# Kernel tuning notes

Hardware: AMD Instinct MI355X
Metric: run time of the kernel (lower is better)

## Reference

```python
import jax, jax.numpy as jnp
import numpy as np

B = 2048       # batch
N = 256        # num_memory_locations
M = 64         # memory_size
U = 512        # num_units
IN = 10        # num_bits_per_vector + 2
SHIFT = 1      # conv_shift_range
CLIP = 20.0


def setup_inputs() -> dict:
    key = jax.random.key(0)
    ks = jax.random.split(key, 20)
    s = 0.05
    A0 = jax.random.uniform(ks[5], (2, B, N), dtype=jnp.float32)
    A0 = A0 / jnp.sum(A0, axis=-1, keepdims=True)  # distribution-like prev attention
    return {
        'x_t':  jax.random.normal(ks[0], (B, IN), dtype=jnp.float32),
        'H0':   jax.random.normal(ks[1], (B, U), dtype=jnp.float32) * s,
        'C0':   jax.random.normal(ks[2], (B, U), dtype=jnp.float32) * s,
        'm0':   jax.random.normal(ks[3], (B, N, M), dtype=jnp.float32) * s,
        'R0':   jax.random.normal(ks[4], (B, M), dtype=jnp.float32) * s,
        'A0':   A0,
        'Wprep': jax.random.normal(ks[6], (M, U), dtype=jnp.float32) * s,
        'bprep': jnp.zeros((U,), dtype=jnp.float32),
        'Wx':   jax.random.normal(ks[7], (IN + U, 4 * U), dtype=jnp.float32) * s,
        'Wh':   jax.random.normal(ks[8], (U, 4 * U), dtype=jnp.float32) * s,
        'bl':   jnp.zeros((4 * U,), dtype=jnp.float32),
        'Wr':   jax.random.normal(ks[9], (U, M + 6), dtype=jnp.float32) * s,
        'br':   jnp.zeros((M + 6,), dtype=jnp.float32),
        'Ww':   jax.random.normal(ks[10], (U, 3 * M + 6), dtype=jnp.float32) * s,
        'bw':   jnp.zeros((3 * M + 6,), dtype=jnp.float32),
        'Wo':   jax.random.normal(ks[11], (U + M, U), dtype=jnp.float32) * s,
        'bo':   jnp.zeros((U,), dtype=jnp.float32),
    }


def _addressing(head, m_tm1, a_tm1):
    # head: (B, >=M+6); m_tm1: (B,N,M); a_tm1: (B,N)
    k = jnp.tanh(head[:, :M])                                   # (B,M)
    beta = jax.nn.softplus(head[:, M])                          # (B,)
    g = jax.nn.sigmoid(head[:, M + 1])                          # (B,)
    s = jax.nn.softmax(head[:, M + 2:M + 2 + 2 * SHIFT + 1], axis=-1)  # (B,3)
    gamma = jax.nn.softplus(head[:, M + 2 + 2 * SHIFT + 1])     # (B,)
    # cosine similarity content addressing
    ip = jnp.einsum('bnm,bm->bn', m_tm1, k)                     # (B,N)
    k_norm = jnp.sqrt(jnp.sum(k * k, axis=1, keepdims=True))    # (B,1)
    m_norm = jnp.sqrt(jnp.sum(m_tm1 * m_tm1, axis=2))           # (B,N)
    K = ip / (k_norm * m_norm + 1e-8)
    w_c = jax.nn.softmax(beta[:, None] * K, axis=1)             # exp/sum == softmax
    w_g = g[:, None] * w_c + (1.0 - g[:, None]) * a_tm1
    # circular convolution: s placed at offsets [0..SHIFT] and [-SHIFT..-1]
    s_full = jnp.concatenate(
        [s[:, :SHIFT + 1], jnp.zeros((s.shape[0], N - (2 * SHIFT + 1)), s.dtype), s[:, -SHIFT:]],
        axis=1)                                                 # (B,N)
    idx = (jnp.arange(N)[:, None] - jnp.arange(N)[None, :]) % N  # (N,N)
    w_conv = jnp.einsum('bij,bj->bi', s_full[:, idx], w_g)       # w[i]=sum_j w_g[j]*s[(i-j)%N]
    w_sharp = w_conv ** gamma[:, None]
    return w_sharp / jnp.sum(w_sharp, axis=1, keepdims=True)


def reference(x_t, H0, C0, m0, R0, A0, Wprep, bprep, Wx, Wh, bl, Wr, br, Ww, bw, Wo, bo):
    # prep from previous reads
    h = R0 @ Wprep + bprep                                      # (B,U)
    # single-layer LSTM controller
    z = jnp.concatenate([x_t, h], axis=1) @ Wx + H0 @ Wh + bl   # (B,4U)
    i, f, g_, o = jnp.split(z, 4, axis=1)
    c_t = jax.nn.sigmoid(f) * C0 + jax.nn.sigmoid(i) * jnp.tanh(g_)
    h = jax.nn.sigmoid(o) * jnp.tanh(c_t)
    h = jnp.clip(h, -CLIP, CLIP)
    # heads
    r_out = h @ Wr + br                                         # (B, M+6)
    w_out = h @ Ww + bw                                         # (B, 3M+6)
    w_read = _addressing(r_out, m0, A0[0])                      # (B,N)
    w_write = _addressing(w_out, m0, A0[1])                     # (B,N)
    # read from OLD memory (as in original)
    R_t = jnp.einsum('bn,bnm->bm', w_read, m0)                  # (B,M)
    # write: erase + add
    del_v = jax.nn.sigmoid(w_out[:, -2 * M:-M])                 # (B,M)
    add_v = jnp.tanh(w_out[:, -M:])                             # (B,M)
    ww = w_write[:, :, None]                                    # (B,N,1)
    m_t = m0 * (1.0 - ww * del_v[:, None, :]) + ww * add_v[:, None, :]
    y_t = jnp.clip(jnp.concatenate([h, R_t], axis=1) @ Wo + bo, -CLIP, CLIP)
    return (y_t, m_t, R_t, w_read, w_write)
```

## Files before the change

kernel.cpp:

```cpp
#include <hip/hip_runtime.h>


using u16   = unsigned short;
using bfrag = __attribute__((ext_vector_type(8))) short;
using f4    = __attribute__((ext_vector_type(4))) float;

__device__ __forceinline__ float bf2f(u16 s){ union{float f;unsigned u;}v; v.u=((unsigned)s)<<16; return v.f; }
__device__ __forceinline__ u16 f2bf(float f){ union{float f;unsigned u;}v; v.f=f; unsigned r=v.u+0x7fffu+((v.u>>16)&1u); return (u16)(r>>16); }
__device__ __forceinline__ float sigm(float x){ return 1.f/(1.f+expf(-x)); }
__device__ __forceinline__ float softplus_(float x){ return fmaxf(x,0.f)+log1pf(expf(-fabsf(x))); }

__device__ __forceinline__ void gld16(const u16* g, u16* l){
    __builtin_amdgcn_global_load_lds((const __attribute__((address_space(1))) unsigned*)g,
                                     (__attribute__((address_space(3))) unsigned*)l, 16, 0, 0);
}

__global__ __launch_bounds__(256) void k_prep(const float* __restrict__ Wx, const float* __restrict__ Wh,
                                              const float* __restrict__ Wr, const float* __restrict__ Ww,
                                              const float* __restrict__ Wo,
                                              const float* __restrict__ x, const float* __restrict__ H0,
                                              const float* __restrict__ R0, const float* __restrict__ Wprep,
                                              const float* __restrict__ bprep,
                                              u16* __restrict__ Wt_lstm, u16* __restrict__ Wt_h,
                                              u16* __restrict__ Wt_o, u16* __restrict__ Abuf){
    __shared__ float t[32][33];
    int bx = blockIdx.x;
    int tx = threadIdx.x & 31, ty = threadIdx.x >> 5;
    if(bx < 2112){
        int n0 = (bx & 63)*32, k0 = (bx >> 6)*32;
        #pragma unroll
        for(int r=0;r<4;r++){
            int k = k0 + ty*4 + r, n = n0 + tx;
            float v;
            if(k < 522)       v = Wx[k*2048 + n];
            else if(k < 1034) v = Wh[(k-522)*2048 + n];
            else              v = 0.f;
            t[ty*4+r][tx] = v;
        }
        __syncthreads();
        #pragma unroll
        for(int r=0;r<4;r++){
            int n = n0 + ty*4 + r, k = k0 + tx;
            int u = n & 511, gate = n >> 9;
            int np = ((u>>4)<<6) + (gate<<4) + (u&15);
            Wt_lstm[np*1056 + k] = f2bf(t[tx][ty*4+r]);
        }
    } else if(bx < 2304){
        int idx = bx - 2112;
        int n0 = (idx % 12)*32, k0 = (idx / 12)*32;
        #pragma unroll
        for(int r=0;r<4;r++){
            int k = k0 + ty*4 + r, n = n0 + tx;
            float v;
            if(n < 70)        v = Wr[k*70 + n];
            else if(n < 268)  v = Ww[k*198 + (n-70)];
            else              v = 0.f;
            t[ty*4+r][tx] = v;
        }
        __syncthreads();
        #pragma unroll
        for(int r=0;r<4;r++){
            int n = n0 + ty*4 + r, k = k0 + tx;
            Wt_h[n*512 + k] = f2bf(t[tx][ty*4+r]);
        }
    } else if(bx < 2592){
        int idx = bx - 2304;
        int n0 = (idx % 16)*32, k0 = (idx / 16)*32;
        #pragma unroll
        for(int r=0;r<4;r++){
            int k = k0 + ty*4 + r, n = n0 + tx;
            t[ty*4+r][tx] = Wo[k*512 + n];
        }
        __syncthreads();
        #pragma unroll
        for(int r=0;r<4;r++){
            int n = n0 + ty*4 + r, k = k0 + tx;
            Wt_o[n*576 + k] = f2bf(t[tx][ty*4+r]);
        }
    } else {
        int flat = (bx - 2592)*256 + threadIdx.x;
        int b = flat >> 9, u = flat & 511;
        u16* Ab = Abuf + (size_t)b*1056;
        float acc = bprep[u];
        const float* r = R0 + b*64;
        #pragma unroll 8
        for(int m=0;m<64;m++) acc += r[m] * Wprep[m*512+u];
        Ab[10+u] = f2bf(acc);
        Ab[522+u] = f2bf(H0[b*512+u]);
        if(u<10) Ab[u] = f2bf(x[b*10+u]);
        if(u<22) Ab[1034+u] = 0;
    }
}

__device__ __forceinline__ void gemm128(const u16* __restrict__ A, int lda,
                                        const u16* __restrict__ Bt, int ldb,
                                        int bm, int bn, int kiters,
                                        u16* Al, u16* Bl, f4 acc[4][4]){
    int tid = threadIdx.x, w = tid>>6, lane = tid&63, quad = lane>>4, l16 = lane&15;
    int wr = w>>1, wc = w&1;
    f4 z4 = {0.f,0.f,0.f,0.f};
    #pragma unroll
    for(int i=0;i<4;i++)
        #pragma unroll
        for(int j=0;j<4;j++) acc[i][j] = z4;
    int rA0 = tid>>2, kc = tid&3;
    int rA1 = rA0 + 64;
    const u16* ga0 = A  + (size_t)(bm+rA0)*lda + kc*8;
    const u16* ga1 = A  + (size_t)(bm+rA1)*lda + kc*8;
    const u16* gb0 = Bt + (size_t)(bn+rA0)*ldb + kc*8;
    const u16* gb1 = Bt + (size_t)(bn+rA1)*ldb + kc*8;
    u16* lA0 = Al + (w*64)*8;
    u16* lA1 = Al + (256 + w*64)*8;
    u16* lB0 = Bl + (w*64)*8;
    u16* lB1 = Bl + (256 + w*64)*8;
    for(int kt=0; kt<kiters; kt++){
        __syncthreads();
        gld16(ga0, lA0); gld16(ga1, lA1);
        gld16(gb0, lB0); gld16(gb1, lB1);
        ga0 += 32; ga1 += 32; gb0 += 32; gb1 += 32;
        __syncthreads();
        bfrag af[4], bf[4];
        #pragma unroll
        for(int i=0;i<4;i++) af[i] = *(const bfrag*)&Al[(wr*64 + i*16 + l16)*32 + quad*8];
        #pragma unroll
        for(int j=0;j<4;j++) bf[j] = *(const bfrag*)&Bl[(wc*64 + j*16 + l16)*32 + quad*8];
        #pragma unroll
        for(int i=0;i<4;i++)
            #pragma unroll
            for(int j=0;j<4;j++)
                acc[i][j] = __builtin_amdgcn_mfma_f32_16x16x32_bf16(af[i], bf[j], acc[i][j], 0, 0, 0);
    }
}

__global__ __launch_bounds__(256) void k_gemm_lstm(const u16* __restrict__ A, const u16* __restrict__ Wt,
                                                   const float* __restrict__ C0, const float* __restrict__ bl,
                                                   u16* __restrict__ A2){
    __shared__ u16 Al[128*32], Bl[128*32];
    f4 acc[4][4];
    int bm = blockIdx.x*128, bn = blockIdx.y*128;
    gemm128(A, 1056, Wt, 1056, bm, bn, 33, Al, Bl, acc);
    int lane = threadIdx.x&63, quad = lane>>4, l16 = lane&15, w = threadIdx.x>>6;
    int wr = w>>1, wc = w&1;
    int u = (((bn + wc*64)>>6)<<4) + l16;
    float bi = bl[u], bff = bl[512+u], bg = bl[1024+u], bo_ = bl[1536+u];
    #pragma unroll
    for(int i=0;i<4;i++){
        #pragma unroll
        for(int r=0;r<4;r++){
            int b = bm + wr*64 + i*16 + quad*4 + r;
            float zi = acc[i][0][r] + bi;
            float zf = acc[i][1][r] + bff;
            float zg = acc[i][2][r] + bg;
            float zo = acc[i][3][r] + bo_;
            float c  = sigm(zf)*C0[b*512+u] + sigm(zi)*tanhf(zg);
            float hv = sigm(zo)*tanhf(c);
            hv = fminf(fmaxf(hv,-20.f),20.f);
            A2[(size_t)b*576 + u] = f2bf(hv);
        }
    }
}

__global__ __launch_bounds__(256) void k_gemm_heads(const u16* __restrict__ A2, const u16* __restrict__ Wt,
                                                    const float* __restrict__ br, const float* __restrict__ bw,
                                                    float* __restrict__ rout, float* __restrict__ wout){
    __shared__ u16 Al[128*32], Bl[128*32];
    f4 acc[4][4];
    int bm = blockIdx.x*128, bn = blockIdx.y*128;
    gemm128(A2, 576, Wt, 512, bm, bn, 16, Al, Bl, acc);
    int lane = threadIdx.x&63, quad = lane>>4, l16 = lane&15, w = threadIdx.x>>6;
    int wr = w>>1, wc = w&1;
    #pragma unroll
    for(int i=0;i<4;i++){
        #pragma unroll
        for(int j=0;j<4;j++){
            int col = bn + wc*64 + j*16 + l16;
            if(col >= 268) continue;
            #pragma unroll
            for(int r=0;r<4;r++){
                int row = bm + wr*64 + i*16 + quad*4 + r;
                float v = acc[i][j][r];
                if(col < 70) rout[(size_t)row*70 + col]        = v + br[col];
                else         wout[(size_t)row*198 + (col-70)]  = v + bw[col-70];
            }
        }
    }
}

__global__ __launch_bounds__(256) void k_gemm_out(const u16* __restrict__ A2, const u16* __restrict__ Wt,
                                                  const float* __restrict__ bo, float* __restrict__ y){
    __shared__ u16 Al[128*32], Bl[128*32];
    f4 acc[4][4];
    int bm = blockIdx.x*128, bn = blockIdx.y*128;
    gemm128(A2, 576, Wt, 576, bm, bn, 18, Al, Bl, acc);
    int lane = threadIdx.x&63, quad = lane>>4, l16 = lane&15, w = threadIdx.x>>6;
    int wr = w>>1, wc = w&1;
    #pragma unroll
    for(int i=0;i<4;i++){
        #pragma unroll
        for(int j=0;j<4;j++){
            int col = bn + wc*64 + j*16 + l16;
            float bias = bo[col];
            #pragma unroll
            for(int r=0;r<4;r++){
                int row = bm + wr*64 + i*16 + quad*4 + r;
                float v = acc[i][j][r] + bias;
                v = fminf(fmaxf(v,-20.f),20.f);
                y[(size_t)row*512 + col] = v;
            }
        }
    }
}

__global__ __launch_bounds__(256, 4) void k_addr(const float* __restrict__ m0, const float* __restrict__ A0,
                                              const float* __restrict__ rout, const float* __restrict__ wout,
                                              u16* __restrict__ A2,
                                              float* __restrict__ out_mt, float* __restrict__ out_rt,
                                              float* __restrict__ out_wr, float* __restrict__ out_ww){
    __shared__ __align__(16) float kk_s[2][64];
    __shared__ float knorm_s[2];
    __shared__ float sc[2][6];
    __shared__ float ipbuf[3][256];
    __shared__ float wgrr[512];
    __shared__ float wsel[2][256];
    __shared__ __align__(16) float dv[64], avv[64];
    __shared__ float wpart[4][6];
    int tid = threadIdx.x, b = blockIdx.x;
    int lane = tid & 63, w = tid >> 6;
    int g = tid >> 4, c = tid & 15, mc = c*4;

    float a0r = A0[b*256 + tid];
    float a1r = A0[524288 + b*256 + tid];

    float4 v[16];
    const float* mb = m0 + (size_t)b*16384;
    #pragma unroll
    for(int i=0;i<16;i++) v[i] = *(const float4*)(mb + i*1024 + tid*4);

    if(tid < 128){
        int hh = tid >> 6, m = lane;
        float kv = tanhf(hh ? wout[b*198 + m] : rout[b*70 + m]);
        kk_s[hh][m] = kv;
        float s2 = kv*kv;
        #pragma unroll
        for(int o=32;o>0;o>>=1) s2 += __shfl_xor(s2, o, 64);
        if(m == 0) knorm_s[hh] = sqrtf(s2);
    } else if(tid < 192){
        int hh = tid - 128;
        if(hh < 2){
            const float* hd = hh ? (wout + b*198) : (rout + b*70);
            sc[hh][0] = softplus_(hd[64]);
            sc[hh][1] = sigm(hd[65]);
            float e0=hd[66], e1=hd[67], e2=hd[68];
            float mx = fmaxf(e0, fmaxf(e1, e2));
            float x0=expf(e0-mx), x1=expf(e1-mx), x2=expf(e2-mx);
            float ssum = x0+x1+x2;
            sc[hh][2]=x0/ssum; sc[hh][3]=x1/ssum; sc[hh][4]=x2/ssum;
            sc[hh][5] = softplus_(hd[69]);
        }
    } else {
        int m = tid - 192;
        dv[m]  = sigm(wout[b*198 + 70 + m]);
        avv[m] = tanhf(wout[b*198 + 134 + m]);
    }
    __syncthreads();

    {
        float4 ka = *(const float4*)&kk_s[0][mc];
        float4 kb = *(const float4*)&kk_s[1][mc];
        float rip0=0.f, rip1=0.f, rssq=0.f;
        #pragma unroll
        for(int i=0;i<16;i++){
            float4 t = v[i];
            float p0 = t.x*ka.x + t.y*ka.y + t.z*ka.z + t.w*ka.w;
            float p1 = t.x*kb.x + t.y*kb.y + t.z*kb.z + t.w*kb.w;
            float ps = t.x*t.x + t.y*t.y + t.z*t.z + t.w*t.w;
            #pragma unroll
            for(int o=1;o<16;o<<=1){
                p0 += __shfl_xor(p0, o);
                p1 += __shfl_xor(p1, o);
                ps += __shfl_xor(ps, o);
            }
            if(c == i){ rip0 = p0; rip1 = p1; rssq = ps; }
        }
        int idx = c*16 + g;
        ipbuf[0][idx] = rip0;
        ipbuf[1][idx] = rip1;
        ipbuf[2][idx] = rssq;
    }
    __syncthreads();
    float ip0 = ipbuf[0][tid], ip1 = ipbuf[1][tid], ssq = ipbuf[2][tid];

    float mn = sqrtf(ssq);
    float K0 = ip0 / (knorm_s[0]*mn + 1e-8f);
    float K1 = ip1 / (knorm_s[1]*mn + 1e-8f);
    float e0 = sc[0][0]*K0, e1 = sc[1][0]*K1;

    float mx0 = e0, mx1 = e1;
    #pragma unroll
    for(int o=32;o>0;o>>=1){ mx0 = fmaxf(mx0, __shfl_xor(mx0,o,64)); mx1 = fmaxf(mx1, __shfl_xor(mx1,o,64)); }
    if(lane == 0){ wpart[w][0] = mx0; wpart[w][1] = mx1; }
    __syncthreads();
    mx0 = fmaxf(fmaxf(wpart[0][0],wpart[1][0]), fmaxf(wpart[2][0],wpart[3][0]));
    mx1 = fmaxf(fmaxf(wpart[0][1],wpart[1][1]), fmaxf(wpart[2][1],wpart[3][1]));
    float p0 = expf(e0-mx0), p1 = expf(e1-mx1);
    float s0 = p0, s1 = p1;
    #pragma unroll
    for(int o=32;o>0;o>>=1){ s0 += __shfl_xor(s0,o,64); s1 += __shfl_xor(s1,o,64); }
    if(lane == 0){ wpart[w][2] = s0; wpart[w][3] = s1; }
    __syncthreads();
    s0 = wpart[0][2]+wpart[1][2]+wpart[2][2]+wpart[3][2];
    s1 = wpart[0][3]+wpart[1][3]+wpart[2][3]+wpart[3][3];
    float wc0 = p0/s0, wc1 = p1/s1;

    float g0 = sc[0][1], g1 = sc[1][1];
    float wg0 = g0*wc0 + (1.f-g0)*a0r;
    float wg1 = g1*wc1 + (1.f-g1)*a1r;
    wgrr[tid] = wg0; wgrr[256+tid] = wg1;
    __syncthreads();
    int nm1 = (tid+255)&255, np1 = (tid+1)&255;
    float conv0 = sc[0][2]*wg0 + sc[0][3]*wgrr[nm1]     + sc[0][4]*wgrr[np1];
    float conv1 = sc[1][2]*wg1 + sc[1][3]*wgrr[256+nm1] + sc[1][4]*wgrr[256+np1];
    conv0 = fmaxf(conv0, 1e-35f);  conv1 = fmaxf(conv1, 1e-35f);
    float wsh0 = expf(sc[0][5]*logf(conv0));
    float wsh1 = expf(sc[1][5]*logf(conv1));
    float t0 = wsh0, t1 = wsh1;
    #pragma unroll
    for(int o=32;o>0;o>>=1){ t0 += __shfl_xor(t0,o,64); t1 += __shfl_xor(t1,o,64); }
    if(lane == 0){ wpart[w][4] = t0; wpart[w][5] = t1; }
    __syncthreads();
    t0 = wpart[0][4]+wpart[1][4]+wpart[2][4]+wpart[3][4];
    t1 = wpart[0][5]+wpart[1][5]+wpart[2][5]+wpart[3][5];
    float w0 = wsh0/t0, w1 = wsh1/t1;
    wsel[0][tid] = w0; wsel[1][tid] = w1;
    out_wr[b*256 + tid] = w0;
    out_ww[b*256 + tid] = w1;
    __syncthreads();

    float r0=0.f, r1=0.f, r2=0.f, r3=0.f;
    {
        float d0=dv[mc], d1=dv[mc+1], d2=dv[mc+2], d3=dv[mc+3];
        float A0v=avv[mc], A1v=avv[mc+1], A2v=avv[mc+2], A3v=avv[mc+3];
        float* outb = out_mt + (size_t)b*16384;
        #pragma unroll
        for(int i=0;i<16;i++){
            int n = i*16 + g;
            float wwv = wsel[1][n], wrv = wsel[0][n];
            float4 t = v[i];
            float4 o;
            o.x = t.x*(1.f - wwv*d0) + wwv*A0v;
            o.y = t.y*(1.f - wwv*d1) + wwv*A1v;
            o.z = t.z*(1.f - wwv*d2) + wwv*A2v;
            o.w = t.w*(1.f - wwv*d3) + wwv*A3v;
            *(float4*)(outb + i*1024 + tid*4) = o;
            r0 += wrv*t.x; r1 += wrv*t.y; r2 += wrv*t.z; r3 += wrv*t.w;
        }
    }
    {
        float* rred = wgrr;
        if(g >= 8){
            rred[(g-8)*64 + mc]   = r0;
            rred[(g-8)*64 + mc+1] = r1;
            rred[(g-8)*64 + mc+2] = r2;
            rred[(g-8)*64 + mc+3] = r3;
        }
        __syncthreads();
        if(g < 8){
            rred[g*64 + mc]   += r0;
            rred[g*64 + mc+1] += r1;
            rred[g*64 + mc+2] += r2;
            rred[g*64 + mc+3] += r3;
        }
        __syncthreads();
        if(tid < 64){
            float rt = 0.f;
            #pragma unroll
            for(int g2=0; g2<8; g2++) rt += rred[g2*64 + tid];
            out_rt[b*64 + tid] = rt;
            A2[(size_t)b*576 + 512 + tid] = f2bf(rt);
        }
    }
}

extern "C" void kernel_launch(void* const* d_in, const int* in_sizes, int n_in,
                              void* d_out, int out_size, void* d_ws, size_t ws_size,
                              hipStream_t stream) {
    const float* x     = (const float*)d_in[0];
    const float* H0    = (const float*)d_in[1];
    const float* C0    = (const float*)d_in[2];
    const float* m0    = (const float*)d_in[3];
    const float* R0    = (const float*)d_in[4];
    const float* A0    = (const float*)d_in[5];
    const float* Wprep = (const float*)d_in[6];
    const float* bprep = (const float*)d_in[7];
    const float* Wx    = (const float*)d_in[8];
    const float* Wh    = (const float*)d_in[9];
    const float* bl    = (const float*)d_in[10];
    const float* Wr    = (const float*)d_in[11];
    const float* br    = (const float*)d_in[12];
    const float* Ww    = (const float*)d_in[13];
    const float* bw    = (const float*)d_in[14];
    const float* Wo    = (const float*)d_in[15];
    const float* bo    = (const float*)d_in[16];

    float* ws = (float*)d_ws;
    u16*   Wt_lstm = (u16*)(ws + 0);
    u16*   Wt_h    = (u16*)(ws + 1081344);
    u16*   Wt_o    = (u16*)(ws + 1179648);
    u16*   Abuf    = (u16*)(ws + 1327104);
    u16*   A2      = (u16*)(ws + 2408448);
    float* rout    =        ws + 2998272;
    float* wout    =        ws + 3141632;

    float* out    = (float*)d_out;
    float* out_y  = out;
    float* out_mt = out + 1048576;
    float* out_rt = out + 34603008;
    float* out_wr = out + 34734080;
    float* out_ww = out + 35258368;

    hipLaunchKernelGGL(k_prep,      dim3(6688), dim3(256), 0, stream,
                       Wx, Wh, Wr, Ww, Wo, x, H0, R0, Wprep, bprep,
                       Wt_lstm, Wt_h, Wt_o, Abuf);
    hipLaunchKernelGGL(k_gemm_lstm, dim3(16,16), dim3(256), 0, stream, Abuf, Wt_lstm, C0, bl, A2);
    hipLaunchKernelGGL(k_gemm_heads, dim3(16,3), dim3(256), 0, stream, A2, Wt_h, br, bw, rout, wout);
    hipLaunchKernelGGL(k_addr,      dim3(2048),  dim3(256), 0, stream, m0, A0, rout, wout, A2,
                       out_mt, out_rt, out_wr, out_ww);
    hipLaunchKernelGGL(k_gemm_out,  dim3(16,4),  dim3(256), 0, stream, A2, Wt_o, bo, out_y);
}
```

Before: 379.9 us.

## Hold memory tile as packed bf16 in registers to raise k_addr occupancy

The k_addr kernel now packs each loaded float4 of memory into two bf16 pairs held in registers, halving register use for the per-thread memory slice, and raises the launch-bounds occupancy hint from 4 to 6 blocks. The ipbuf scratch is also padded (stride 17) to avoid LDS bank conflicts on the transposed write. This trades precision: the memory values used for the similarity, the read and the erase/add update are rounded to bf16, so m_t loses exactness for positions with near-zero write weight, which may exceed tolerance.

```diff
diff --git a/kernel.cpp b/kernel.cpp
--- a/kernel.cpp
+++ b/kernel.cpp
@@ -7,6 +7,8 @@
 
 __device__ __forceinline__ float bf2f(u16 s){ union{float f;unsigned u;}v; v.u=((unsigned)s)<<16; return v.f; }
 __device__ __forceinline__ u16 f2bf(float f){ union{float f;unsigned u;}v; v.f=f; unsigned r=v.u+0x7fffu+((v.u>>16)&1u); return (u16)(r>>16); }
+__device__ __forceinline__ void bfpair(unsigned pr, float&a, float&b){ union{float f;unsigned u;}x,y; x.u=pr<<16; y.u=pr&0xffff0000u; a=x.f; b=y.f; }
+__device__ __forceinline__ unsigned packbf(float a, float b){ return (unsigned)f2bf(a) | ((unsigned)f2bf(b)<<16); }
 __device__ __forceinline__ float sigm(float x){ return 1.f/(1.f+expf(-x)); }
 __device__ __forceinline__ float softplus_(float x){ return fmaxf(x,0.f)+log1pf(expf(-fabsf(x))); }
 
@@ -211,7 +213,7 @@
     }
 }
 
-__global__ __launch_bounds__(256, 4) void k_addr(const float* __restrict__ m0, const float* __restrict__ A0,
+__global__ __launch_bounds__(256, 6) void k_addr(const float* __restrict__ m0, const float* __restrict__ A0,
                                               const float* __restrict__ rout, const float* __restrict__ wout,
                                               u16* __restrict__ A2,
                                               float* __restrict__ out_mt, float* __restrict__ out_rt,
@@ -219,7 +221,7 @@
     __shared__ __align__(16) float kk_s[2][64];
     __shared__ float knorm_s[2];
     __shared__ float sc[2][6];
-    __shared__ float ipbuf[3][256];
+    __shared__ float ipbuf[3][272];
     __shared__ float wgrr[512];
     __shared__ float wsel[2][256];
     __shared__ __align__(16) float dv[64], avv[64];
@@ -231,10 +233,14 @@
     float a0r = A0[b*256 + tid];
     float a1r = A0[524288 + b*256 + tid];
 
-    float4 v[16];
+    unsigned vp0[16], vp1[16];
     const float* mb = m0 + (size_t)b*16384;
     #pragma unroll
-    for(int i=0;i<16;i++) v[i] = *(const float4*)(mb + i*1024 + tid*4);
+    for(int i=0;i<16;i++){
+        float4 v = *(const float4*)(mb + i*1024 + tid*4);
+        vp0[i] = packbf(v.x, v.y);
+        vp1[i] = packbf(v.z, v.w);
+    }
 
     if(tid < 128){
         int hh = tid >> 6, m = lane;
@@ -270,10 +276,12 @@
         float rip0=0.f, rip1=0.f, rssq=0.f;
         #pragma unroll
         for(int i=0;i<16;i++){
-            float4 t = v[i];
-            float p0 = t.x*ka.x + t.y*ka.y + t.z*ka.z + t.w*ka.w;
-            float p1 = t.x*kb.x + t.y*kb.y + t.z*kb.z + t.w*kb.w;
-            float ps = t.x*t.x + t.y*t.y + t.z*t.z + t.w*t.w;
+            float v0,v1,v2,v3;
+            bfpair(vp0[i], v0, v1);
+            bfpair(vp1[i], v2, v3);
+            float p0 = v0*ka.x + v1*ka.y + v2*ka.z + v3*ka.w;
+            float p1 = v0*kb.x + v1*kb.y + v2*kb.z + v3*kb.w;
+            float ps = v0*v0 + v1*v1 + v2*v2 + v3*v3;
             #pragma unroll
             for(int o=1;o<16;o<<=1){
                 p0 += __shfl_xor(p0, o);
@@ -282,13 +290,14 @@
             }
             if(c == i){ rip0 = p0; rip1 = p1; rssq = ps; }
         }
-        int idx = c*16 + g;
-        ipbuf[0][idx] = rip0;
-        ipbuf[1][idx] = rip1;
-        ipbuf[2][idx] = rssq;
-    }
-    __syncthreads();
-    float ip0 = ipbuf[0][tid], ip1 = ipbuf[1][tid], ssq = ipbuf[2][tid];
+        int slot = c*17 + g;
+        ipbuf[0][slot] = rip0;
+        ipbuf[1][slot] = rip1;
+        ipbuf[2][slot] = rssq;
+    }
+    __syncthreads();
+    int rslot = tid + (tid>>4);
+    float ip0 = ipbuf[0][rslot], ip1 = ipbuf[1][rslot], ssq = ipbuf[2][rslot];
 
     float mn = sqrtf(ssq);
     float K0 = ip0 / (knorm_s[0]*mn + 1e-8f);
@@ -345,14 +354,16 @@
         for(int i=0;i<16;i++){
             int n = i*16 + g;
             float wwv = wsel[1][n], wrv = wsel[0][n];
-            float4 t = v[i];
+            float v0,v1,v2,v3;
+            bfpair(vp0[i], v0, v1);
+            bfpair(vp1[i], v2, v3);
             float4 o;
-            o.x = t.x*(1.f - wwv*d0) + wwv*A0v;
-            o.y = t.y*(1.f - wwv*d1) + wwv*A1v;
-            o.z = t.z*(1.f - wwv*d2) + wwv*A2v;
-            o.w = t.w*(1.f - wwv*d3) + wwv*A3v;
+            o.x = v0*(1.f - wwv*d0) + wwv*A0v;
+            o.y = v1*(1.f - wwv*d1) + wwv*A1v;
+            o.z = v2*(1.f - wwv*d2) + wwv*A2v;
+            o.w = v3*(1.f - wwv*d3) + wwv*A3v;
             *(float4*)(outb + i*1024 + tid*4) = o;
-            r0 += wrv*t.x; r1 += wrv*t.y; r2 += wrv*t.z; r3 += wrv*t.w;
+            r0 += wrv*v0; r1 += wrv*v1; r2 += wrv*v2; r3 += wrv*v3;
         }
     }
     {
```

Result: slower. 422.5 us (+11.2%).

## Use 512 threads per block in addressing kernel, one head per half

Applied to the files above, without the earlier changes.

Doubles the k_addr block size to 512 threads. Each thread now holds 8 float4 rows of memory instead of 16, and each half of the block computes the addressing chain for one head (read or write), so the per-thread dual-head work becomes single-head. The inner-product buffer is padded against bank conflicts, and the read-vector reduction goes through a dedicated 32x64 shared array. The goal is fewer registers per thread and more latency hiding on the memory-bound 128 MB read/write, at the cost of a longer final 32-way reduction and more threads per block.

```diff
diff --git a/kernel.cpp b/kernel.cpp
--- a/kernel.cpp
+++ b/kernel.cpp
@@ -211,7 +211,7 @@
     }
 }
 
-__global__ __launch_bounds__(256, 4) void k_addr(const float* __restrict__ m0, const float* __restrict__ A0,
+__global__ __launch_bounds__(512, 2) void k_addr(const float* __restrict__ m0, const float* __restrict__ A0,
                                               const float* __restrict__ rout, const float* __restrict__ wout,
                                               u16* __restrict__ A2,
                                               float* __restrict__ out_mt, float* __restrict__ out_rt,
@@ -219,47 +219,50 @@
     __shared__ __align__(16) float kk_s[2][64];
     __shared__ float knorm_s[2];
     __shared__ float sc[2][6];
-    __shared__ float ipbuf[3][256];
+    __shared__ float ipbuf[3][272];
     __shared__ float wgrr[512];
     __shared__ float wsel[2][256];
     __shared__ __align__(16) float dv[64], avv[64];
-    __shared__ float wpart[4][6];
+    __shared__ float wpart[8][3];
+    __shared__ __align__(16) float rred[32][64];
     int tid = threadIdx.x, b = blockIdx.x;
     int lane = tid & 63, w = tid >> 6;
     int g = tid >> 4, c = tid & 15, mc = c*4;
 
-    float a0r = A0[b*256 + tid];
-    float a1r = A0[524288 + b*256 + tid];
-
-    float4 v[16];
+    int hh = tid >> 8, rr = tid & 255;
+    float ar = A0[hh*524288 + b*256 + rr];
+
+    float4 v[8];
     const float* mb = m0 + (size_t)b*16384;
     #pragma unroll
-    for(int i=0;i<16;i++) v[i] = *(const float4*)(mb + i*1024 + tid*4);
+    for(int i=0;i<8;i++) v[i] = *(const float4*)(mb + i*2048 + tid*4);
 
     if(tid < 128){
-        int hh = tid >> 6, m = lane;
-        float kv = tanhf(hh ? wout[b*198 + m] : rout[b*70 + m]);
-        kk_s[hh][m] = kv;
+        int h2 = tid >> 6, m = lane;
+        float kv = tanhf(h2 ? wout[b*198 + m] : rout[b*70 + m]);
+        kk_s[h2][m] = kv;
         float s2 = kv*kv;
         #pragma unroll
         for(int o=32;o>0;o>>=1) s2 += __shfl_xor(s2, o, 64);
-        if(m == 0) knorm_s[hh] = sqrtf(s2);
+        if(m == 0) knorm_s[h2] = sqrtf(s2);
     } else if(tid < 192){
-        int hh = tid - 128;
-        if(hh < 2){
-            const float* hd = hh ? (wout + b*198) : (rout + b*70);
-            sc[hh][0] = softplus_(hd[64]);
-            sc[hh][1] = sigm(hd[65]);
+        int h2 = tid - 128;
+        if(h2 < 2){
+            const float* hd = h2 ? (wout + b*198) : (rout + b*70);
+            sc[h2][0] = softplus_(hd[64]);
+            sc[h2][1] = sigm(hd[65]);
             float e0=hd[66], e1=hd[67], e2=hd[68];
             float mx = fmaxf(e0, fmaxf(e1, e2));
             float x0=expf(e0-mx), x1=expf(e1-mx), x2=expf(e2-mx);
             float ssum = x0+x1+x2;
-            sc[hh][2]=x0/ssum; sc[hh][3]=x1/ssum; sc[hh][4]=x2/ssum;
-            sc[hh][5] = softplus_(hd[69]);
-        }
-    } else {
+            sc[h2][2]=x0/ssum; sc[h2][3]=x1/ssum; sc[h2][4]=x2/ssum;
+            sc[h2][5] = softplus_(hd[69]);
+        }
+    } else if(tid < 256){
         int m = tid - 192;
         dv[m]  = sigm(wout[b*198 + 70 + m]);
+    } else if(tid < 320){
+        int m = tid - 256;
         avv[m] = tanhf(wout[b*198 + 134 + m]);
     }
     __syncthreads();
@@ -267,9 +270,8 @@
     {
         float4 ka = *(const float4*)&kk_s[0][mc];
         float4 kb = *(const float4*)&kk_s[1][mc];
-        float rip0=0.f, rip1=0.f, rssq=0.f;
-        #pragma unroll
-        for(int i=0;i<16;i++){
+        #pragma unroll
+        for(int i=0;i<8;i++){
             float4 t = v[i];
             float p0 = t.x*ka.x + t.y*ka.y + t.z*ka.z + t.w*ka.w;
             float p1 = t.x*kb.x + t.y*kb.y + t.z*kb.z + t.w*kb.w;
@@ -280,60 +282,58 @@
                 p1 += __shfl_xor(p1, o);
                 ps += __shfl_xor(ps, o);
             }
-            if(c == i){ rip0 = p0; rip1 = p1; rssq = ps; }
-        }
-        int idx = c*16 + g;
-        ipbuf[0][idx] = rip0;
-        ipbuf[1][idx] = rip1;
-        ipbuf[2][idx] = rssq;
-    }
-    __syncthreads();
-    float ip0 = ipbuf[0][tid], ip1 = ipbuf[1][tid], ssq = ipbuf[2][tid];
-
+            if(c == i){
+                int n = i*32 + g;
+                int slot = n + (n>>4);
+                ipbuf[0][slot] = p0;
+                ipbuf[1][slot] = p1;
+                ipbuf[2][slot] = ps;
+            }
+        }
+    }
+    __syncthreads();
+
+    int rslot = rr + (rr>>4);
+    float ip  = ipbuf[hh][rslot];
+    float ssq = ipbuf[2][rslot];
     float mn = sqrtf(ssq);
-    float K0 = ip0 / (knorm_s[0]*mn + 1e-8f);
-    float K1 = ip1 / (knorm_s[1]*mn + 1e-8f);
-    float e0 = sc[0][0]*K0, e1 = sc[1][0]*K1;
-
-    float mx0 = e0, mx1 = e1;
-    #pragma unroll
-    for(int o=32;o>0;o>>=1){ mx0 = fmaxf(mx0, __shfl_xor(mx0,o,64)); mx1 = fmaxf(mx1, __shfl_xor(mx1,o,64)); }
-    if(lane == 0){ wpart[w][0] = mx0; wpart[w][1] = mx1; }
-    __syncthreads();
-    mx0 = fmaxf(fmaxf(wpart[0][0],wpart[1][0]), fmaxf(wpart[2][0],wpart[3][0]));
-    mx1 = fmaxf(fmaxf(wpart[0][1],wpart[1][1]), fmaxf(wpart[2][1],wpart[3][1]));
-    float p0 = expf(e0-mx0), p1 = expf(e1-mx1);
-    float s0 = p0, s1 = p1;
-    #pragma unroll
-    for(int o=32;o>0;o>>=1){ s0 += __shfl_xor(s0,o,64); s1 += __shfl_xor(s1,o,64); }
-    if(lane == 0){ wpart[w][2] = s0; wpart[w][3] = s1; }
-    __syncthreads();
-    s0 = wpart[0][2]+wpart[1][2]+wpart[2][2]+wpart[3][2];
-    s1 = wpart[0][3]+wpart[1][3]+wpart[2][3]+wpart[3][3];
-    float wc0 = p0/s0, wc1 = p1/s1;
-
-    float g0 = sc[0][1], g1 = sc[1][1];
-    float wg0 = g0*wc0 + (1.f-g0)*a0r;
-    float wg1 = g1*wc1 + (1.f-g1)*a1r;
-    wgrr[tid] = wg0; wgrr[256+tid] = wg1;
-    __syncthreads();
-    int nm1 = (tid+255)&255, np1 = (tid+1)&255;
-    float conv0 = sc[0][2]*wg0 + sc[0][3]*wgrr[nm1]     + sc[0][4]*wgrr[np1];
-    float conv1 = sc[1][2]*wg1 + sc[1][3]*wgrr[256+nm1] + sc[1][4]*wgrr[256+np1];
-    conv0 = fmaxf(conv0, 1e-35f);  conv1 = fmaxf(conv1, 1e-35f);
-    float wsh0 = expf(sc[0][5]*logf(conv0));
-    float wsh1 = expf(sc[1][5]*logf(conv1));
-    float t0 = wsh0, t1 = wsh1;
-    #pragma unroll
-    for(int o=32;o>0;o>>=1){ t0 += __shfl_xor(t0,o,64); t1 += __shfl_xor(t1,o,64); }
-    if(lane == 0){ wpart[w][4] = t0; wpart[w][5] = t1; }
-    __syncthreads();
-    t0 = wpart[0][4]+wpart[1][4]+wpart[2][4]+wpart[3][4];
-    t1 = wpart[0][5]+wpart[1][5]+wpart[2][5]+wpart[3][5];
-    float w0 = wsh0/t0, w1 = wsh1/t1;
-    wsel[0][tid] = w0; wsel[1][tid] = w1;
-    out_wr[b*256 + tid] = w0;
-    out_ww[b*256 + tid] = w1;
+    float K = ip / (knorm_s[hh]*mn + 1e-8f);
+    float e = sc[hh][0]*K;
+
+    int wb = hh*4;
+    float mx = e;
+    #pragma unroll
+    for(int o=32;o>0;o>>=1) mx = fmaxf(mx, __shfl_xor(mx,o,64));
+    if(lane == 0) wpart[w][0] = mx;
+    __syncthreads();
+    mx = fmaxf(fmaxf(wpart[wb][0],wpart[wb+1][0]), fmaxf(wpart[wb+2][0],wpart[wb+3][0]));
+    float p = expf(e-mx);
+    float s = p;
+    #pragma unroll
+    for(int o=32;o>0;o>>=1) s += __shfl_xor(s,o,64);
+    if(lane == 0) wpart[w][1] = s;
+    __syncthreads();
+    s = wpart[wb][1]+wpart[wb+1][1]+wpart[wb+2][1]+wpart[wb+3][1];
+    float wc = p/s;
+
+    float gg = sc[hh][1];
+    float wg = gg*wc + (1.f-gg)*ar;
+    wgrr[tid] = wg;
+    __syncthreads();
+    int base = hh<<8;
+    float conv = sc[hh][2]*wg + sc[hh][3]*wgrr[base + ((rr+255)&255)]
+                              + sc[hh][4]*wgrr[base + ((rr+1)&255)];
+    conv = fmaxf(conv, 1e-35f);
+    float wsh = expf(sc[hh][5]*logf(conv));
+    float t0 = wsh;
+    #pragma unroll
+    for(int o=32;o>0;o>>=1) t0 += __shfl_xor(t0,o,64);
+    if(lane == 0) wpart[w][2] = t0;
+    __syncthreads();
+    t0 = wpart[wb][2]+wpart[wb+1][2]+wpart[wb+2][2]+wpart[wb+3][2];
+    float wfin = wsh/t0;
+    wsel[hh][rr] = wfin;
+    (hh ? out_ww : out_wr)[b*256 + rr] = wfin;
     __syncthreads();
 
     float r0=0.f, r1=0.f, r2=0.f, r3=0.f;
@@ -342,8 +342,8 @@
         float A0v=avv[mc], A1v=avv[mc+1], A2v=avv[mc+2], A3v=avv[mc+3];
         float* outb = out_mt + (size_t)b*16384;
         #pragma unroll
-        for(int i=0;i<16;i++){
-            int n = i*16 + g;
+        for(int i=0;i<8;i++){
+            int n = i*32 + g;
             float wwv = wsel[1][n], wrv = wsel[0][n];
             float4 t = v[i];
             float4 o;
@@ -351,30 +351,18 @@
             o.y = t.y*(1.f - wwv*d1) + wwv*A1v;
             o.z = t.z*(1.f - wwv*d2) + wwv*A2v;
             o.w = t.w*(1.f - wwv*d3) + wwv*A3v;
-            *(float4*)(outb + i*1024 + tid*4) = o;
+            *(float4*)(outb + i*2048 + tid*4) = o;
             r0 += wrv*t.x; r1 += wrv*t.y; r2 += wrv*t.z; r3 += wrv*t.w;
         }
     }
     {
-        float* rred = wgrr;
-        if(g >= 8){
-            rred[(g-8)*64 + mc]   = r0;
-            rred[(g-8)*64 + mc+1] = r1;
-            rred[(g-8)*64 + mc+2] = r2;
-            rred[(g-8)*64 + mc+3] = r3;
-        }
-        __syncthreads();
-        if(g < 8){
-            rred[g*64 + mc]   += r0;
-            rred[g*64 + mc+1] += r1;
-            rred[g*64 + mc+2] += r2;
-            rred[g*64 + mc+3] += r3;
-        }
+        float4 rv; rv.x=r0; rv.y=r1; rv.z=r2; rv.w=r3;
+        *(float4*)&rred[g][mc] = rv;
         __syncthreads();
         if(tid < 64){
             float rt = 0.f;
             #pragma unroll
-            for(int g2=0; g2<8; g2++) rt += rred[g2*64 + tid];
+            for(int g2=0; g2<32; g2++) rt += rred[g2][tid];
             out_rt[b*64 + tid] = rt;
             A2[(size_t)b*576 + 512 + tid] = f2bf(rt);
         }
@@ -423,7 +411,7 @@
                        Wt_lstm, Wt_h, Wt_o, Abuf);
     hipLaunchKernelGGL(k_gemm_lstm, dim3(16,16), dim3(256), 0, stream, Abuf, Wt_lstm, C0, bl, A2);
     hipLaunchKernelGGL(k_gemm_heads, dim3(16,3), dim3(256), 0, stream, A2, Wt_h, br, bw, rout, wout);
-    hipLaunchKernelGGL(k_addr,      dim3(2048),  dim3(256), 0, stream, m0, A0, rout, wout, A2,
+    hipLaunchKernelGGL(k_addr,      dim3(2048),  dim3(512), 0, stream, m0, A0, rout, wout, A2,
                        out_mt, out_rt, out_wr, out_ww);
     hipLaunchKernelGGL(k_gemm_out,  dim3(16,4),  dim3(256), 0, stream, A2, Wt_o, bo, out_y);
 }
```

Measured after the change: 374.2 us. No clear change (-1.5%).
